# Optimization experiments

Measured on AMD Instinct MI355X. Metric: run time of the kernel, lower is better.

## Reference

```python
import jax, jax.numpy as jnp
import numpy as np

NUM_NODES = 100000
EMBED_DIM = 64
NUM_LAYERS = 3
NUM_EDGES = 1250000


def setup_inputs() -> dict:
    key = jax.random.key(0)
    k1, k2 = jax.random.split(key)
    edge_index = jax.random.randint(k1, (2, NUM_EDGES), 0, NUM_NODES, dtype=jnp.int64)
    # xavier_uniform for Embedding weight: bound = sqrt(6/(fan_in+fan_out))
    bound = float(np.sqrt(6.0 / (NUM_NODES + EMBED_DIM)))
    emb = jax.random.uniform(k2, (NUM_NODES, EMBED_DIM), dtype=jnp.float32,
                             minval=-bound, maxval=bound)
    return {"edge_index": edge_index, "emb": emb}


def reference(edge_index, emb):
    row, col = edge_index[0], edge_index[1]
    num_nodes = emb.shape[0]
    # degree from source index (bincount over row)
    deg = jax.ops.segment_sum(jnp.ones_like(row, dtype=emb.dtype), row,
                              num_segments=num_nodes)
    deg_inv_sqrt = jnp.where(deg > 0, jax.lax.rsqrt(jnp.maximum(deg, 1.0)) * jnp.where(deg > 0, 1.0, 0.0), 0.0)
    deg_inv_sqrt = jnp.where(deg > 0, deg ** -0.5, 0.0)

    x = emb
    acc = emb  # running sum of all_embeddings
    for _ in range(NUM_LAYERS):
        m = deg_inv_sqrt[row][:, None] * x[col]           # [E, D] gather + scale
        x = jax.ops.segment_sum(m, row, num_segments=num_nodes)  # scatter-add
        x = x * deg_inv_sqrt[:, None]
        acc = acc + x
    return acc / (NUM_LAYERS + 1)
```

## Files before the change

### kernel.cpp

```cpp
#include <hip/hip_runtime.h>
#include <math.h>

#define N_NODES 100000
#define DIM 64
#define N_EDGES 1250000
#define SCAN_BLOCKS 256
#define RPB 128
#define NB_BUCKETS ((N_NODES + RPB - 1) / RPB)
#define NBLK_B 128
#define CNT_N (NB_BUCKETS * NBLK_B)
#define CAP 2048

typedef unsigned short ushort_t;
typedef unsigned int uint_t;

__device__ __forceinline__ float hlo(uint_t u) {
    return (float)__builtin_bit_cast(_Float16, (ushort_t)(u & 0xFFFFu));
}
__device__ __forceinline__ float hhi(uint_t u) {
    return (float)__builtin_bit_cast(_Float16, (ushort_t)(u >> 16));
}
__device__ __forceinline__ uint_t f2h(float f) {
    return (uint_t)__builtin_bit_cast(ushort_t, (_Float16)f);
}

__global__ void conv_kernel(const float* __restrict__ emb, ushort_t* __restrict__ embh, int n8) {
    int i = blockIdx.x * blockDim.x + threadIdx.x;
    if (i < n8) {
        float4 a = reinterpret_cast<const float4*>(emb)[2 * i];
        float4 b = reinterpret_cast<const float4*>(emb)[2 * i + 1];
        uint4 w;
        w.x = f2h(a.x) | (f2h(a.y) << 16);
        w.y = f2h(a.z) | (f2h(a.w) << 16);
        w.z = f2h(b.x) | (f2h(b.y) << 16);
        w.w = f2h(b.z) | (f2h(b.w) << 16);
        reinterpret_cast<uint4*>(embh)[i] = w;
    }
}

__global__ void bucket_hist_kernel(const int* __restrict__ row, int* __restrict__ cnt, int E) {
    __shared__ int h[NB_BUCKETS];
    for (int i = threadIdx.x; i < NB_BUCKETS; i += blockDim.x) h[i] = 0;
    __syncthreads();
    int blk = blockIdx.x;
    int per = (E + (int)gridDim.x - 1) / (int)gridDim.x;
    int lo = blk * per, hi = min(lo + per, E);
    for (int e = lo + (int)threadIdx.x; e < hi; e += blockDim.x)
        atomicAdd(&h[row[e] >> 7], 1);
    __syncthreads();
    for (int b = threadIdx.x; b < NB_BUCKETS; b += blockDim.x)
        cnt[b * NBLK_B + blk] = h[b];
}

__global__ void partial_kernel(const int* __restrict__ in, int* __restrict__ blocksum,
                               int N, int chunk) {
    __shared__ int sh[256];
    int b = blockIdx.x;
    int lo = b * chunk, hi = min(lo + chunk, N);
    int s = 0;
    for (int i = lo + (int)threadIdx.x; i < hi; i += 256) s += in[i];
    sh[threadIdx.x] = s;
    __syncthreads();
    for (int off = 128; off > 0; off >>= 1) {
        if ((int)threadIdx.x < off) sh[threadIdx.x] += sh[threadIdx.x + off];
        __syncthreads();
    }
    if (threadIdx.x == 0) blocksum[b] = sh[0];
}

__global__ void scan_small_kernel(int* __restrict__ blocksum, int* __restrict__ out, int N) {
    __shared__ int sh[SCAN_BLOCKS];
    int t = threadIdx.x;
    int v = blocksum[t];
    sh[t] = v;
    __syncthreads();
    for (int off = 1; off < SCAN_BLOCKS; off <<= 1) {
        int u = (t >= off) ? sh[t - off] : 0;
        __syncthreads();
        sh[t] += u;
        __syncthreads();
    }
    blocksum[t] = sh[t] - v;
    if (t == SCAN_BLOCKS - 1) out[N] = sh[SCAN_BLOCKS - 1];
}

__global__ void scan_emit_kernel(const int* __restrict__ in, const int* __restrict__ blocksum,
                                 int* __restrict__ out, int N, int chunk) {
    __shared__ int sh[256];
    int b = blockIdx.x;
    int t = threadIdx.x;
    int lo = b * chunk, hi = min(lo + chunk, N);
    int running = blocksum[b];
    for (int base = lo; base < hi; base += 256) {
        int i = base + t;
        int d = (i < hi) ? in[i] : 0;
        sh[t] = d;
        __syncthreads();
        for (int off = 1; off < 256; off <<= 1) {
            int u = (t >= off) ? sh[t - off] : 0;
            __syncthreads();
            sh[t] += u;
            __syncthreads();
        }
        if (i < hi) out[i] = running + (sh[t] - d);
        running += sh[255];
        __syncthreads();
    }
}

__global__ void bucket_scatter_kernel(const int* __restrict__ row, const int* __restrict__ col,
                                      const int* __restrict__ slot_off,
                                      int* __restrict__ pairs, int E) {
    __shared__ int cur[NB_BUCKETS];
    int blk = blockIdx.x;
    for (int b = threadIdx.x; b < NB_BUCKETS; b += blockDim.x)
        cur[b] = slot_off[b * NBLK_B + blk];
    __syncthreads();
    int per = (E + (int)gridDim.x - 1) / (int)gridDim.x;
    int lo = blk * per, hi = min(lo + per, E);
    for (int e = lo + (int)threadIdx.x; e < hi; e += blockDim.x) {
        int r = row[e], c = col[e];
        int pos = atomicAdd(&cur[r >> 7], 1);
        pairs[pos] = ((r & (RPB - 1)) << 17) | c;
    }
}

__global__ void __launch_bounds__(256) bucket_csr_kernel(
        const int* __restrict__ slot_off, const int* __restrict__ pairs,
        int* __restrict__ row_ptr, float* __restrict__ dis,
        int* __restrict__ csr_col, int E) {
    __shared__ int pk[CAP];
    __shared__ int csr_lds[CAP];
    __shared__ int deg_loc[RPB];
    __shared__ int scan_loc[RPB];
    __shared__ int cur_loc[RPB];
    int b = blockIdx.x;
    int t = threadIdx.x;
    int start = slot_off[b * NBLK_B];
    int end = slot_off[(b + 1) * NBLK_B];
    int cnt = end - start;
    bool fits = (cnt <= CAP);

    if (t < RPB) deg_loc[t] = 0;
    if (fits) {
        for (int i = t; i < cnt; i += 256) pk[i] = pairs[start + i];
    }
    __syncthreads();
    for (int i = t; i < cnt; i += 256) {
        int p = fits ? pk[i] : pairs[start + i];
        atomicAdd(&deg_loc[p >> 17], 1);
    }
    __syncthreads();
    int d = (t < RPB) ? deg_loc[t] : 0;
    if (t < RPB) scan_loc[t] = d;
    __syncthreads();
    for (int off = 1; off < RPB; off <<= 1) {
        int v = (t < RPB && t >= off) ? scan_loc[t - off] : 0;
        __syncthreads();
        if (t < RPB) scan_loc[t] += v;
        __syncthreads();
    }
    if (t < RPB) {
        int exc = scan_loc[t] - d;
        cur_loc[t] = exc;
        int rg = b * RPB + t;
        if (rg < N_NODES) {
            row_ptr[rg] = start + exc;
            dis[rg] = (d > 0) ? (float)(1.0 / sqrt((double)d)) : 0.0f;
        }
    }
    __syncthreads();
    for (int i = t; i < cnt; i += 256) {
        int p = fits ? pk[i] : pairs[start + i];
        int pos = atomicAdd(&cur_loc[p >> 17], 1);
        int c = p & 0x1FFFF;
        if (fits) csr_lds[pos] = c;
        else      csr_col[start + pos] = c;
    }
    __syncthreads();
    if (fits) {
        for (int i = t; i < cnt; i += 256) csr_col[start + i] = csr_lds[i];
    }
    if (b == NB_BUCKETS - 1 && t == 0) row_ptr[N_NODES] = E;
}

__global__ void gather_kernel(const int* __restrict__ row_ptr, const int* __restrict__ csr_col,
                              const float* __restrict__ dis,
                              const ushort_t* __restrict__ x_old, ushort_t* __restrict__ x_new,
                              int Npair) {
    int wid = (int)((blockIdx.x * (size_t)blockDim.x + threadIdx.x) >> 6);
    if (wid >= Npair) return;
    int lane = threadIdx.x & 63;
    int sub = lane >> 5;
    int l5 = lane & 31;
    int g = l5 >> 3;
    int l = l5 & 7;
    int node = wid * 2 + sub;

    int start = row_ptr[node];
    int end = row_ptr[node + 1];

    float acc[8];
    #pragma unroll
    for (int k = 0; k < 8; ++k) acc[k] = 0.f;

    int e = start + g;
    for (; e + 4 < end; e += 8) {
        int c0 = csr_col[e];
        int c1 = csr_col[e + 4];
        uint4 v0 = *reinterpret_cast<const uint4*>(&x_old[(size_t)c0 * DIM + l * 8]);
        uint4 v1 = *reinterpret_cast<const uint4*>(&x_old[(size_t)c1 * DIM + l * 8]);
        acc[0] += hlo(v0.x); acc[1] += hhi(v0.x);
        acc[2] += hlo(v0.y); acc[3] += hhi(v0.y);
        acc[4] += hlo(v0.z); acc[5] += hhi(v0.z);
        acc[6] += hlo(v0.w); acc[7] += hhi(v0.w);
        acc[0] += hlo(v1.x); acc[1] += hhi(v1.x);
        acc[2] += hlo(v1.y); acc[3] += hhi(v1.y);
        acc[4] += hlo(v1.z); acc[5] += hhi(v1.z);
        acc[6] += hlo(v1.w); acc[7] += hhi(v1.w);
    }
    if (e < end) {
        int c0 = csr_col[e];
        uint4 v0 = *reinterpret_cast<const uint4*>(&x_old[(size_t)c0 * DIM + l * 8]);
        acc[0] += hlo(v0.x); acc[1] += hhi(v0.x);
        acc[2] += hlo(v0.y); acc[3] += hhi(v0.y);
        acc[4] += hlo(v0.z); acc[5] += hhi(v0.z);
        acc[6] += hlo(v0.w); acc[7] += hhi(v0.w);
    }

    #pragma unroll
    for (int off = 8; off <= 16; off <<= 1) {
        #pragma unroll
        for (int k = 0; k < 8; ++k) acc[k] += __shfl_xor(acc[k], off, 64);
    }

    if (g == 0) {
        float s = dis[node];
        float s2 = s * s;
        uint4 w;
        w.x = f2h(acc[0] * s2) | (f2h(acc[1] * s2) << 16);
        w.y = f2h(acc[2] * s2) | (f2h(acc[3] * s2) << 16);
        w.z = f2h(acc[4] * s2) | (f2h(acc[5] * s2) << 16);
        w.w = f2h(acc[6] * s2) | (f2h(acc[7] * s2) << 16);
        *reinterpret_cast<uint4*>(&x_new[(size_t)node * DIM + l * 8]) = w;
    }
}

__global__ void combine_kernel(const ushort_t* __restrict__ e0, const ushort_t* __restrict__ x1,
                               const ushort_t* __restrict__ x2, const ushort_t* __restrict__ x3,
                               float* __restrict__ out, int n8) {
    int i = blockIdx.x * blockDim.x + threadIdx.x;
    if (i < n8) {
        uint4 a = reinterpret_cast<const uint4*>(e0)[i];
        uint4 b = reinterpret_cast<const uint4*>(x1)[i];
        uint4 c = reinterpret_cast<const uint4*>(x2)[i];
        uint4 d = reinterpret_cast<const uint4*>(x3)[i];
        float4 r0, r1;
        r0.x = (hlo(a.x) + hlo(b.x) + hlo(c.x) + hlo(d.x)) * 0.25f;
        r0.y = (hhi(a.x) + hhi(b.x) + hhi(c.x) + hhi(d.x)) * 0.25f;
        r0.z = (hlo(a.y) + hlo(b.y) + hlo(c.y) + hlo(d.y)) * 0.25f;
        r0.w = (hhi(a.y) + hhi(b.y) + hhi(c.y) + hhi(d.y)) * 0.25f;
        r1.x = (hlo(a.z) + hlo(b.z) + hlo(c.z) + hlo(d.z)) * 0.25f;
        r1.y = (hhi(a.z) + hhi(b.z) + hhi(c.z) + hhi(d.z)) * 0.25f;
        r1.z = (hlo(a.w) + hlo(b.w) + hlo(c.w) + hlo(d.w)) * 0.25f;
        r1.w = (hhi(a.w) + hhi(b.w) + hhi(c.w) + hhi(d.w)) * 0.25f;
        reinterpret_cast<float4*>(out)[2 * i] = r0;
        reinterpret_cast<float4*>(out)[2 * i + 1] = r1;
    }
}

extern "C" void kernel_launch(void* const* d_in, const int* in_sizes, int n_in,
                              void* d_out, int out_size, void* d_ws, size_t ws_size,
                              hipStream_t stream) {
    const int* edge = (const int*)d_in[0];
    const int* row = edge;
    const int* col = edge + N_EDGES;
    const float* emb = (const float*)d_in[1];
    float* out = (float*)d_out;

    char* ws = (char*)d_ws;
    size_t off = 0;
    auto alloc = [&](size_t bytes) {
        char* p = ws + off;
        off += (bytes + 255) & ~(size_t)255;
        return p;
    };
    int*      row_ptr  = (int*)alloc(((size_t)N_NODES + 1) * sizeof(int));
    float*    dis      = (float*)alloc((size_t)N_NODES * sizeof(float));
    int*      blocksum = (int*)alloc((size_t)SCAN_BLOCKS * sizeof(int));
    int*      cnt      = (int*)alloc((size_t)CNT_N * sizeof(int));
    int*      slot_off = (int*)alloc(((size_t)CNT_N + 1) * sizeof(int));
    int*      csr_col  = (int*)alloc((size_t)N_EDGES * sizeof(int));
    ushort_t* embh     = (ushort_t*)alloc((size_t)N_NODES * DIM * sizeof(ushort_t));
    ushort_t* x1       = (ushort_t*)alloc((size_t)N_NODES * DIM * sizeof(ushort_t));
    ushort_t* x2       = (ushort_t*)alloc((size_t)N_NODES * DIM * sizeof(ushort_t));
    ushort_t* x3       = (ushort_t*)alloc((size_t)N_NODES * DIM * sizeof(ushort_t));
    int*      pairs    = (int*)x2;

    const int gather_blocks = (N_NODES / 2 * 64) / 256;
    const int chunk = (CNT_N + SCAN_BLOCKS - 1) / SCAN_BLOCKS;
    const int n8 = N_NODES * DIM / 8;

    conv_kernel<<<(n8 + 255) / 256, 256, 0, stream>>>(emb, embh, n8);
    bucket_hist_kernel<<<NBLK_B, 256, 0, stream>>>(row, cnt, N_EDGES);
    partial_kernel<<<SCAN_BLOCKS, 256, 0, stream>>>(cnt, blocksum, CNT_N, chunk);
    scan_small_kernel<<<1, SCAN_BLOCKS, 0, stream>>>(blocksum, slot_off, CNT_N);
    scan_emit_kernel<<<SCAN_BLOCKS, 256, 0, stream>>>(cnt, blocksum, slot_off, CNT_N, chunk);
    bucket_scatter_kernel<<<NBLK_B, 256, 0, stream>>>(row, col, slot_off, pairs, N_EDGES);
    bucket_csr_kernel<<<NB_BUCKETS, 256, 0, stream>>>(slot_off, pairs, row_ptr, dis, csr_col, N_EDGES);

    gather_kernel<<<gather_blocks, 256, 0, stream>>>(row_ptr, csr_col, dis, embh, x1, N_NODES / 2);
    gather_kernel<<<gather_blocks, 256, 0, stream>>>(row_ptr, csr_col, dis, x1, x2, N_NODES / 2);
    gather_kernel<<<gather_blocks, 256, 0, stream>>>(row_ptr, csr_col, dis, x2, x3, N_NODES / 2);

    combine_kernel<<<(n8 + 255) / 256, 256, 0, stream>>>(embh, x1, x2, x3, out, n8);
}
```

Before: 152.9 us.

## Fuse conversion with histogram and final combine into last gather layer

Merges the fp32-to-fp16 conversion into the bucket histogram launch and folds the final averaging into the third gather layer, which drops two launches and the x3 buffer round trip. CSR column entries are stored pre-multiplied as byte offsets, so the gather loop skips the index arithmetic. Half-precision accumulation now uses the fdot2 builtin against unit vectors in place of separate converts and adds. The final layer reads three more fp16 rows per node inside the gather, so that kernel does a little more memory traffic.

```diff
diff --git a/kernel.cpp b/kernel.cpp
--- a/kernel.cpp
+++ b/kernel.cpp
@@ -13,6 +13,7 @@
 
 typedef unsigned short ushort_t;
 typedef unsigned int uint_t;
+typedef _Float16 h2 __attribute__((ext_vector_type(2)));
 
 __device__ __forceinline__ float hlo(uint_t u) {
     return (float)__builtin_bit_cast(_Float16, (ushort_t)(u & 0xFFFFu));
@@ -24,32 +25,47 @@
     return (uint_t)__builtin_bit_cast(ushort_t, (_Float16)f);
 }
 
-__global__ void conv_kernel(const float* __restrict__ emb, ushort_t* __restrict__ embh, int n8) {
-    int i = blockIdx.x * blockDim.x + threadIdx.x;
-    if (i < n8) {
-        float4 a = reinterpret_cast<const float4*>(emb)[2 * i];
-        float4 b = reinterpret_cast<const float4*>(emb)[2 * i + 1];
-        uint4 w;
-        w.x = f2h(a.x) | (f2h(a.y) << 16);
-        w.y = f2h(a.z) | (f2h(a.w) << 16);
-        w.z = f2h(b.x) | (f2h(b.y) << 16);
-        w.w = f2h(b.z) | (f2h(b.w) << 16);
-        reinterpret_cast<uint4*>(embh)[i] = w;
-    }
-}
-
-__global__ void bucket_hist_kernel(const int* __restrict__ row, int* __restrict__ cnt, int E) {
+__device__ __forceinline__ void dacc(float& a0, float& a1, uint_t u) {
+#if __has_builtin(__builtin_amdgcn_fdot2)
+    h2 h = __builtin_bit_cast(h2, u);
+    const h2 e0 = {(_Float16)1.0f, (_Float16)0.0f};
+    const h2 e1 = {(_Float16)0.0f, (_Float16)1.0f};
+    a0 = __builtin_amdgcn_fdot2(h, e0, a0, false);
+    a1 = __builtin_amdgcn_fdot2(h, e1, a1, false);
+#else
+    a0 += hlo(u);
+    a1 += hhi(u);
+#endif
+}
+
+__global__ void conv_hist_kernel(const float* __restrict__ emb, ushort_t* __restrict__ embh,
+                                 int n8, const int* __restrict__ row,
+                                 int* __restrict__ cnt, int E) {
     __shared__ int h[NB_BUCKETS];
-    for (int i = threadIdx.x; i < NB_BUCKETS; i += blockDim.x) h[i] = 0;
-    __syncthreads();
-    int blk = blockIdx.x;
-    int per = (E + (int)gridDim.x - 1) / (int)gridDim.x;
-    int lo = blk * per, hi = min(lo + per, E);
-    for (int e = lo + (int)threadIdx.x; e < hi; e += blockDim.x)
-        atomicAdd(&h[row[e] >> 7], 1);
-    __syncthreads();
-    for (int b = threadIdx.x; b < NB_BUCKETS; b += blockDim.x)
-        cnt[b * NBLK_B + blk] = h[b];
+    if (blockIdx.x < NBLK_B) {
+        for (int i = threadIdx.x; i < NB_BUCKETS; i += blockDim.x) h[i] = 0;
+        __syncthreads();
+        int blk = blockIdx.x;
+        int per = (E + NBLK_B - 1) / NBLK_B;
+        int lo = blk * per, hi = min(lo + per, E);
+        for (int e = lo + (int)threadIdx.x; e < hi; e += blockDim.x)
+            atomicAdd(&h[row[e] >> 7], 1);
+        __syncthreads();
+        for (int b = threadIdx.x; b < NB_BUCKETS; b += blockDim.x)
+            cnt[b * NBLK_B + blk] = h[b];
+    } else {
+        int i = (blockIdx.x - NBLK_B) * blockDim.x + threadIdx.x;
+        if (i < n8) {
+            float4 a = reinterpret_cast<const float4*>(emb)[2 * i];
+            float4 b = reinterpret_cast<const float4*>(emb)[2 * i + 1];
+            uint4 w;
+            w.x = f2h(a.x) | (f2h(a.y) << 16);
+            w.y = f2h(a.z) | (f2h(a.w) << 16);
+            w.z = f2h(b.x) | (f2h(b.y) << 16);
+            w.w = f2h(b.z) | (f2h(b.w) << 16);
+            reinterpret_cast<uint4*>(embh)[i] = w;
+        }
+    }
 }
 
 __global__ void partial_kernel(const int* __restrict__ in, int* __restrict__ blocksum,
@@ -173,7 +189,7 @@
     for (int i = t; i < cnt; i += 256) {
         int p = fits ? pk[i] : pairs[start + i];
         int pos = atomicAdd(&cur_loc[p >> 17], 1);
-        int c = p & 0x1FFFF;
+        int c = (p & 0x1FFFF) << 7;
         if (fits) csr_lds[pos] = c;
         else      csr_col[start + pos] = c;
     }
@@ -184,9 +200,12 @@
     if (b == NB_BUCKETS - 1 && t == 0) row_ptr[N_NODES] = E;
 }
 
+template <int MODE>
 __global__ void gather_kernel(const int* __restrict__ row_ptr, const int* __restrict__ csr_col,
                               const float* __restrict__ dis,
                               const ushort_t* __restrict__ x_old, ushort_t* __restrict__ x_new,
+                              const ushort_t* __restrict__ e0, const ushort_t* __restrict__ x1,
+                              const ushort_t* __restrict__ x2, float* __restrict__ out,
                               int Npair) {
     int wid = (int)((blockIdx.x * (size_t)blockDim.x + threadIdx.x) >> 6);
     if (wid >= Npair) return;
@@ -200,32 +219,29 @@
     int start = row_ptr[node];
     int end = row_ptr[node + 1];
 
+    const char* xb = (const char*)x_old;
+    int lb = l * 16;
+
     float acc[8];
     #pragma unroll
     for (int k = 0; k < 8; ++k) acc[k] = 0.f;
 
     int e = start + g;
     for (; e + 4 < end; e += 8) {
-        int c0 = csr_col[e];
-        int c1 = csr_col[e + 4];
-        uint4 v0 = *reinterpret_cast<const uint4*>(&x_old[(size_t)c0 * DIM + l * 8]);
-        uint4 v1 = *reinterpret_cast<const uint4*>(&x_old[(size_t)c1 * DIM + l * 8]);
-        acc[0] += hlo(v0.x); acc[1] += hhi(v0.x);
-        acc[2] += hlo(v0.y); acc[3] += hhi(v0.y);
-        acc[4] += hlo(v0.z); acc[5] += hhi(v0.z);
-        acc[6] += hlo(v0.w); acc[7] += hhi(v0.w);
-        acc[0] += hlo(v1.x); acc[1] += hhi(v1.x);
-        acc[2] += hlo(v1.y); acc[3] += hhi(v1.y);
-        acc[4] += hlo(v1.z); acc[5] += hhi(v1.z);
-        acc[6] += hlo(v1.w); acc[7] += hhi(v1.w);
+        int o0 = csr_col[e];
+        int o1 = csr_col[e + 4];
+        uint4 v0 = *reinterpret_cast<const uint4*>(xb + o0 + lb);
+        uint4 v1 = *reinterpret_cast<const uint4*>(xb + o1 + lb);
+        dacc(acc[0], acc[1], v0.x); dacc(acc[2], acc[3], v0.y);
+        dacc(acc[4], acc[5], v0.z); dacc(acc[6], acc[7], v0.w);
+        dacc(acc[0], acc[1], v1.x); dacc(acc[2], acc[3], v1.y);
+        dacc(acc[4], acc[5], v1.z); dacc(acc[6], acc[7], v1.w);
     }
     if (e < end) {
-        int c0 = csr_col[e];
-        uint4 v0 = *reinterpret_cast<const uint4*>(&x_old[(size_t)c0 * DIM + l * 8]);
-        acc[0] += hlo(v0.x); acc[1] += hhi(v0.x);
-        acc[2] += hlo(v0.y); acc[3] += hhi(v0.y);
-        acc[4] += hlo(v0.z); acc[5] += hhi(v0.z);
-        acc[6] += hlo(v0.w); acc[7] += hhi(v0.w);
+        int o0 = csr_col[e];
+        uint4 v0 = *reinterpret_cast<const uint4*>(xb + o0 + lb);
+        dacc(acc[0], acc[1], v0.x); dacc(acc[2], acc[3], v0.y);
+        dacc(acc[4], acc[5], v0.z); dacc(acc[6], acc[7], v0.w);
     }
 
     #pragma unroll
@@ -237,35 +253,31 @@
     if (g == 0) {
         float s = dis[node];
         float s2 = s * s;
-        uint4 w;
-        w.x = f2h(acc[0] * s2) | (f2h(acc[1] * s2) << 16);
-        w.y = f2h(acc[2] * s2) | (f2h(acc[3] * s2) << 16);
-        w.z = f2h(acc[4] * s2) | (f2h(acc[5] * s2) << 16);
-        w.w = f2h(acc[6] * s2) | (f2h(acc[7] * s2) << 16);
-        *reinterpret_cast<uint4*>(&x_new[(size_t)node * DIM + l * 8]) = w;
-    }
-}
-
-__global__ void combine_kernel(const ushort_t* __restrict__ e0, const ushort_t* __restrict__ x1,
-                               const ushort_t* __restrict__ x2, const ushort_t* __restrict__ x3,
-                               float* __restrict__ out, int n8) {
-    int i = blockIdx.x * blockDim.x + threadIdx.x;
-    if (i < n8) {
-        uint4 a = reinterpret_cast<const uint4*>(e0)[i];
-        uint4 b = reinterpret_cast<const uint4*>(x1)[i];
-        uint4 c = reinterpret_cast<const uint4*>(x2)[i];
-        uint4 d = reinterpret_cast<const uint4*>(x3)[i];
-        float4 r0, r1;
-        r0.x = (hlo(a.x) + hlo(b.x) + hlo(c.x) + hlo(d.x)) * 0.25f;
-        r0.y = (hhi(a.x) + hhi(b.x) + hhi(c.x) + hhi(d.x)) * 0.25f;
-        r0.z = (hlo(a.y) + hlo(b.y) + hlo(c.y) + hlo(d.y)) * 0.25f;
-        r0.w = (hhi(a.y) + hhi(b.y) + hhi(c.y) + hhi(d.y)) * 0.25f;
-        r1.x = (hlo(a.z) + hlo(b.z) + hlo(c.z) + hlo(d.z)) * 0.25f;
-        r1.y = (hhi(a.z) + hhi(b.z) + hhi(c.z) + hhi(d.z)) * 0.25f;
-        r1.z = (hlo(a.w) + hlo(b.w) + hlo(c.w) + hlo(d.w)) * 0.25f;
-        r1.w = (hhi(a.w) + hhi(b.w) + hhi(c.w) + hhi(d.w)) * 0.25f;
-        reinterpret_cast<float4*>(out)[2 * i] = r0;
-        reinterpret_cast<float4*>(out)[2 * i + 1] = r1;
+        if (MODE != 2) {
+            uint4 w;
+            w.x = f2h(acc[0] * s2) | (f2h(acc[1] * s2) << 16);
+            w.y = f2h(acc[2] * s2) | (f2h(acc[3] * s2) << 16);
+            w.z = f2h(acc[4] * s2) | (f2h(acc[5] * s2) << 16);
+            w.w = f2h(acc[6] * s2) | (f2h(acc[7] * s2) << 16);
+            *reinterpret_cast<uint4*>(&x_new[(size_t)node * DIM + l * 8]) = w;
+        } else {
+            size_t ob = (size_t)node * (DIM * 2) + lb;
+            uint4 ea  = *reinterpret_cast<const uint4*>((const char*)e0 + ob);
+            uint4 u1  = *reinterpret_cast<const uint4*>((const char*)x1 + ob);
+            uint4 u2  = *reinterpret_cast<const uint4*>((const char*)x2 + ob);
+            float4 r0, r1;
+            r0.x = (hlo(ea.x) + hlo(u1.x) + hlo(u2.x) + acc[0] * s2) * 0.25f;
+            r0.y = (hhi(ea.x) + hhi(u1.x) + hhi(u2.x) + acc[1] * s2) * 0.25f;
+            r0.z = (hlo(ea.y) + hlo(u1.y) + hlo(u2.y) + acc[2] * s2) * 0.25f;
+            r0.w = (hhi(ea.y) + hhi(u1.y) + hhi(u2.y) + acc[3] * s2) * 0.25f;
+            r1.x = (hlo(ea.z) + hlo(u1.z) + hlo(u2.z) + acc[4] * s2) * 0.25f;
+            r1.y = (hhi(ea.z) + hhi(u1.z) + hhi(u2.z) + acc[5] * s2) * 0.25f;
+            r1.z = (hlo(ea.w) + hlo(u1.w) + hlo(u2.w) + acc[6] * s2) * 0.25f;
+            r1.w = (hhi(ea.w) + hhi(u1.w) + hhi(u2.w) + acc[7] * s2) * 0.25f;
+            size_t oo = (size_t)node * DIM + l * 8;
+            *reinterpret_cast<float4*>(&out[oo]) = r0;
+            *reinterpret_cast<float4*>(&out[oo + 4]) = r1;
+        }
     }
 }
 
@@ -294,24 +306,23 @@
     ushort_t* embh     = (ushort_t*)alloc((size_t)N_NODES * DIM * sizeof(ushort_t));
     ushort_t* x1       = (ushort_t*)alloc((size_t)N_NODES * DIM * sizeof(ushort_t));
     ushort_t* x2       = (ushort_t*)alloc((size_t)N_NODES * DIM * sizeof(ushort_t));
-    ushort_t* x3       = (ushort_t*)alloc((size_t)N_NODES * DIM * sizeof(ushort_t));
     int*      pairs    = (int*)x2;
 
     const int gather_blocks = (N_NODES / 2 * 64) / 256;
     const int chunk = (CNT_N + SCAN_BLOCKS - 1) / SCAN_BLOCKS;
     const int n8 = N_NODES * DIM / 8;
 
-    conv_kernel<<<(n8 + 255) / 256, 256, 0, stream>>>(emb, embh, n8);
-    bucket_hist_kernel<<<NBLK_B, 256, 0, stream>>>(row, cnt, N_EDGES);
+    conv_hist_kernel<<<NBLK_B + (n8 + 255) / 256, 256, 0, stream>>>(emb, embh, n8, row, cnt, N_EDGES);
     partial_kernel<<<SCAN_BLOCKS, 256, 0, stream>>>(cnt, blocksum, CNT_N, chunk);
     scan_small_kernel<<<1, SCAN_BLOCKS, 0, stream>>>(blocksum, slot_off, CNT_N);
     scan_emit_kernel<<<SCAN_BLOCKS, 256, 0, stream>>>(cnt, blocksum, slot_off, CNT_N, chunk);
     bucket_scatter_kernel<<<NBLK_B, 256, 0, stream>>>(row, col, slot_off, pairs, N_EDGES);
     bucket_csr_kernel<<<NB_BUCKETS, 256, 0, stream>>>(slot_off, pairs, row_ptr, dis, csr_col, N_EDGES);
 
-    gather_kernel<<<gather_blocks, 256, 0, stream>>>(row_ptr, csr_col, dis, embh, x1, N_NODES / 2);
-    gather_kernel<<<gather_blocks, 256, 0, stream>>>(row_ptr, csr_col, dis, x1, x2, N_NODES / 2);
-    gather_kernel<<<gather_blocks, 256, 0, stream>>>(row_ptr, csr_col, dis, x2, x3, N_NODES / 2);
-
-    combine_kernel<<<(n8 + 255) / 256, 256, 0, stream>>>(embh, x1, x2, x3, out, n8);
-}
+    gather_kernel<0><<<gather_blocks, 256, 0, stream>>>(row_ptr, csr_col, dis, embh, x1,
+                                                        nullptr, nullptr, nullptr, nullptr, N_NODES / 2);
+    gather_kernel<1><<<gather_blocks, 256, 0, stream>>>(row_ptr, csr_col, dis, x1, x2,
+                                                        nullptr, nullptr, nullptr, nullptr, N_NODES / 2);
+    gather_kernel<2><<<gather_blocks, 256, 0, stream>>>(row_ptr, csr_col, dis, x2, nullptr,
+                                                        embh, x1, x2, out, N_NODES / 2);
+}
```

Result: faster. 143.0 us (-6.4%).
